# Kernel optimization log

Hardware: AMD Instinct MI355X
Metric: run time of the kernel (lower is better)

## Reference

```python
import jax, jax.numpy as jnp
import numpy as np
from jax import lax

SCALES = [4, 8, 16]
K_PER_SCALE = 4


def setup_inputs() -> dict:
    key = jax.random.key(0)
    B, N, D = 32, 4096, 384  # N = 64*64 perfect square
    features = jax.random.normal(key, (B, N, D), dtype=jnp.float32)
    return {"features": features}


def _kmeans_pp(feats, key, k):
    """k-means++ seeding on feats [N, D]; returns [k, D] centers.

    Faithful to torch version: first center uniform random, subsequent
    centers sampled with prob proportional to squared min distance
    (cdist is euclidean; probs = min_dist**2 == squared distance).
    Incremental min over squared distances is equivalent to recomputing
    cdist to all centers and taking the min each iteration.
    """
    N = feats.shape[0]
    k0, k1 = jax.random.split(key)
    idx0 = jax.random.randint(k0, (), 0, N)
    c0 = feats[idx0]  # [D]
    min_sq = jnp.sum((feats - c0) ** 2, axis=1)  # [N] squared dists

    def step(min_sq, kk):
        probs = min_sq / (min_sq.sum() + 1e-8)
        idx = jax.random.categorical(kk, jnp.log(probs + 1e-12))
        c = feats[idx]
        d = jnp.sum((feats - c) ** 2, axis=1)
        return jnp.minimum(min_sq, d), c

    keys = jax.random.split(k1, k - 1)
    _, rest = lax.scan(step, min_sq, keys)  # rest: [k-1, D]
    return jnp.concatenate([c0[None], rest], axis=0)


def reference(features):
    B, N, D = features.shape
    H = W = int(np.sqrt(N))
    x = features.reshape(B, H, W, D)
    base = jax.random.key(42)
    all_slots = []
    for si, s in enumerate(SCALES):
        # adaptive_avg_pool2d with H divisible by s == block mean
        pooled = x.reshape(B, s, H // s, s, W // s, D).mean(axis=(2, 4))  # [B,s,s,D]
        flat = pooled.reshape(B, s * s, D)
        bkeys = jax.random.split(jax.random.fold_in(base, si), B)
        cents = jax.vmap(lambda f, kk: _kmeans_pp(f, kk, K_PER_SCALE))(flat, bkeys)
        all_slots.append(cents)  # [B, k, D]
    return jnp.concatenate(all_slots, axis=1)  # [B, len(scales)*k, D]
```

## Files before the change

kernel.cpp:

```cpp
#include <hip/hip_runtime.h>
#include <stdint.h>

#define D_ 384
#define NPTS 4096
#define W4_OFF 0
#define W8_OFF 196608
#define W16_OFF 983040

__device__ __forceinline__ void tf_round(uint32_t& x0, uint32_t& x1, int r) {
  x0 += x1;
  x1 = (x1 << r) | (x1 >> (32 - r));
  x1 ^= x0;
}

__device__ void tf2x32(uint32_t k0, uint32_t k1, uint32_t x0, uint32_t x1,
                       uint32_t& y0, uint32_t& y1) {
  uint32_t ks2 = k0 ^ k1 ^ 0x1BD11BDAu;
  x0 += k0; x1 += k1;
  tf_round(x0, x1, 13); tf_round(x0, x1, 15); tf_round(x0, x1, 26); tf_round(x0, x1, 6);
  x0 += k1; x1 += ks2 + 1u;
  tf_round(x0, x1, 17); tf_round(x0, x1, 29); tf_round(x0, x1, 16); tf_round(x0, x1, 24);
  x0 += ks2; x1 += k0 + 2u;
  tf_round(x0, x1, 13); tf_round(x0, x1, 15); tf_round(x0, x1, 26); tf_round(x0, x1, 6);
  x0 += k0; x1 += k1 + 3u;
  tf_round(x0, x1, 17); tf_round(x0, x1, 29); tf_round(x0, x1, 16); tf_round(x0, x1, 24);
  x0 += k1; x1 += ks2 + 4u;
  tf_round(x0, x1, 13); tf_round(x0, x1, 15); tf_round(x0, x1, 26); tf_round(x0, x1, 6);
  x0 += ks2; x1 += k0 + 5u;
  y0 = x0; y1 = x1;
}

__global__ __launch_bounds__(384) void pool16_kernel(const float* __restrict__ feats,
                                                     float* __restrict__ ws) {
  int blk = blockIdx.x;
  int b = blk >> 6;
  int cell = ((blk & 63) << 2) + threadIdx.y;
  int q = threadIdx.x;
  int ch = cell >> 4, cw = cell & 15;
  const float* fb = feats + (size_t)b * NPTS * D_;
  float ax = 0.f, ay = 0.f, az = 0.f, aw = 0.f;
  #pragma unroll
  for (int dh = 0; dh < 4; ++dh) {
    int h = ch * 4 + dh;
    #pragma unroll
    for (int dw = 0; dw < 4; ++dw) {
      int w = cw * 4 + dw;
      float4 v = *(const float4*)(fb + ((size_t)(h * 64 + w)) * D_ + q * 4);
      ax += v.x; ay += v.y; az += v.z; aw += v.w;
    }
  }
  float4 o = { ax * (1.f/16.f), ay * (1.f/16.f), az * (1.f/16.f), aw * (1.f/16.f) };
  *(float4*)(ws + W16_OFF + ((size_t)(b * 256 + cell)) * D_ + q * 4) = o;
}

__global__ __launch_bounds__(256) void pool_rest_kernel(float* __restrict__ ws) {
  int gid = blockIdx.x * 256 + threadIdx.x;
  if (gid < 196608) {
    int q = gid % 96;
    int c8 = (gid / 96) & 63;
    int b = gid / (96 * 64);
    int p = c8 >> 3, r = c8 & 7;
    const float4* w16b = (const float4*)(ws + W16_OFF + (size_t)b * 256 * D_);
    float ax = 0.f, ay = 0.f, az = 0.f, aw = 0.f;
    #pragma unroll
    for (int a = 0; a < 2; ++a)
      #pragma unroll
      for (int c = 0; c < 2; ++c) {
        int cell = (p * 2 + a) * 16 + (r * 2 + c);
        float4 v = w16b[(size_t)cell * 96 + q];
        ax += v.x; ay += v.y; az += v.z; aw += v.w;
      }
    float4 o = { ax * 0.25f, ay * 0.25f, az * 0.25f, aw * 0.25f };
    *(float4*)(ws + W8_OFF + ((size_t)(b * 64 + c8)) * D_ + q * 4) = o;
  } else {
    int idx = gid - 196608;
    int q = idx % 96;
    int c4 = (idx / 96) & 15;
    int b = idx / (96 * 16);
    int p = c4 >> 2, r = c4 & 3;
    const float4* w16b = (const float4*)(ws + W16_OFF + (size_t)b * 256 * D_);
    float ax = 0.f, ay = 0.f, az = 0.f, aw = 0.f;
    #pragma unroll
    for (int a = 0; a < 2; ++a)
      #pragma unroll
      for (int c = 0; c < 2; ++c) {
        int p8 = p * 2 + a, r8 = r * 2 + c;
        float bx = 0.f, by = 0.f, bz = 0.f, bw = 0.f;
        #pragma unroll
        for (int a2 = 0; a2 < 2; ++a2)
          #pragma unroll
          for (int c2 = 0; c2 < 2; ++c2) {
            int cell = (p8 * 2 + a2) * 16 + (r8 * 2 + c2);
            float4 v = w16b[(size_t)cell * 96 + q];
            bx += v.x; by += v.y; bz += v.z; bw += v.w;
          }
        bx *= 0.25f; by *= 0.25f; bz *= 0.25f; bw *= 0.25f;
        ax += bx; ay += by; az += bz; aw += bw;
      }
    float4 o = { ax * 0.25f, ay * 0.25f, az * 0.25f, aw * 0.25f };
    *(float4*)(ws + W4_OFF + ((size_t)(b * 16 + c4)) * D_ + q * 4) = o;
  }
}

__global__ __launch_bounds__(512) void kmeans_kernel(const float* __restrict__ ws,
                                                     float* __restrict__ out) {
  int blk = blockIdx.x;
  int si = blk >> 5;
  int b  = blk & 31;
  int n  = (si == 0) ? 16 : (si == 1) ? 64 : 256;

  const float* pooled;
  if (si == 0)      pooled = ws + W4_OFF  + (size_t)b * 16  * D_;
  else if (si == 1) pooled = ws + W8_OFF  + (size_t)b * 64  * D_;
  else              pooled = ws + W16_OFF + (size_t)b * 256 * D_;
  float* ob = out + ((size_t)b * 12 + si * 4) * D_;

  __shared__ __align__(16) float4 csh4[98];
  __shared__ float minsq[256];
  __shared__ uint32_t skey[3][2];
  __shared__ int sidx0;
  __shared__ float wmaxv[4];
  __shared__ int   wmaxi[4];

  int tid  = threadIdx.x;
  int row  = tid >> 1;
  int part = tid & 1;
  int lane = tid & 63;
  int wv   = tid >> 6;

  float4 xr[48];
  if (row < n) {
    const float4* rp = (const float4*)(pooled + (size_t)row * D_ + part * 192);
    #pragma unroll
    for (int k = 0; k < 48; ++k) xr[k] = rp[k];
  }
  if (tid < 256) minsq[tid] = 0.f;

  if (tid < 64) {
    uint32_t f0, f1, bk0, bk1, r0, r1, s0, s1, e0, e1;
    tf2x32(0u, 42u, 0u, (uint32_t)si, f0, f1);
    tf2x32(f0, f1, 0u, (uint32_t)b, bk0, bk1);
    uint32_t cC = (tid < 3) ? 1u : 0u;
    tf2x32(bk0, bk1, 0u, cC, r0, r1);
    uint32_t cD = (tid < 3) ? (uint32_t)tid : 1u;
    tf2x32(r0, r1, 0u, cD, s0, s1);
    tf2x32(s0, s1, 0u, 0u, e0, e1);
    if (tid < 3) { skey[tid][0] = s0; skey[tid][1] = s1; }
    else if (tid == 3) sidx0 = (int)((e0 ^ e1) & (uint32_t)(n - 1));
  }
  __syncthreads();

  int s = sidx0;
  if (row == s) {
    float4* cb = csh4 + part * 49;
    float4* op = (float4*)(ob + part * 192);
    #pragma unroll
    for (int k = 0; k < 48; ++k) { cb[k] = xr[k]; op[k] = xr[k]; }
  }
  __syncthreads();

  if (row < n) {
    float acc = 0.f;
    #pragma unroll
    for (int k = 0; k < 48; ++k) {
      float4 c4 = csh4[part * 49 + k];
      float dx = xr[k].x - c4.x, dy = xr[k].y - c4.y;
      float dz = xr[k].z - c4.z, dw = xr[k].w - c4.w;
      acc += dx * dx; acc += dy * dy; acc += dz * dz; acc += dw * dw;
    }
    acc += __shfl_xor(acc, 1);
    if (part == 0) minsq[row] = acc;
  }
  __syncthreads();

  const float TINY = __uint_as_float(0x00800000u);

  #pragma unroll 1
  for (int t = 0; t < 3; ++t) {
    if (tid < 256) {
      float z = -1e30f;
      if (tid < n) {
        float m = minsq[tid];
        uint32_t y0, y1;
        tf2x32(skey[t][0], skey[t][1], 0u, (uint32_t)tid, y0, y1);
        uint32_t bits = y0 ^ y1;
        float f = __uint_as_float((bits >> 9) | 0x3F800000u) - 1.0f;
        float u = (f > 0.f) ? f : TINY;
        z = -__logf(-__logf(u)) + __logf(m);
      }
      float bv = z; int bi = tid;
      #pragma unroll
      for (int m2 = 1; m2 < 64; m2 <<= 1) {
        float ov = __shfl_xor(bv, m2);
        int   oi = __shfl_xor(bi, m2);
        if (ov > bv || (ov == bv && oi < bi)) { bv = ov; bi = oi; }
      }
      if (lane == 0) { wmaxv[wv] = bv; wmaxi[wv] = bi; }
    }
    __syncthreads();

    float cv = wmaxv[0]; int ci = wmaxi[0];
    #pragma unroll
    for (int w2 = 1; w2 < 4; ++w2)
      if (wmaxv[w2] > cv || (wmaxv[w2] == cv && wmaxi[w2] < ci)) { cv = wmaxv[w2]; ci = wmaxi[w2]; }
    s = ci;

    if (row == s) {
      float4* op = (float4*)(ob + (size_t)(t + 1) * D_ + part * 192);
      float4* cb = csh4 + part * 49;
      #pragma unroll
      for (int k = 0; k < 48; ++k) { op[k] = xr[k]; if (t < 2) cb[k] = xr[k]; }
    }
    if (t < 2) {
      __syncthreads();
      if (row < n) {
        float acc = 0.f;
        #pragma unroll
        for (int k = 0; k < 48; ++k) {
          float4 c4 = csh4[part * 49 + k];
          float dx = xr[k].x - c4.x, dy = xr[k].y - c4.y;
          float dz = xr[k].z - c4.z, dw = xr[k].w - c4.w;
          acc += dx * dx; acc += dy * dy; acc += dz * dz; acc += dw * dw;
        }
        acc += __shfl_xor(acc, 1);
        if (part == 0) minsq[row] = fminf(minsq[row], acc);
      }
      __syncthreads();
    }
  }
}

extern "C" void kernel_launch(void* const* d_in, const int* in_sizes, int n_in,
                              void* d_out, int out_size, void* d_ws, size_t ws_size,
                              hipStream_t stream) {
  const float* feats = (const float*)d_in[0];
  float* out = (float*)d_out;
  float* ws  = (float*)d_ws;

  pool16_kernel<<<2048, dim3(96, 4, 1), 0, stream>>>(feats, ws);
  pool_rest_kernel<<<960, 256, 0, stream>>>(ws);
  kmeans_kernel<<<96, 512, 0, stream>>>(ws, out);
}
```

Baseline: 63.52 us.

## Transpose pooled features to dim-major layout and split rows across four threads

Replaces the coarser-scale pooling kernel with one that transposes the 16x16 pooled features through shared memory into a dimension-major layout and builds the 8x8 and 4x4 pools from that tile. The k-means kernel now runs 1024 threads with four threads per point, each holding 96 scalars, and reads the transposed data so consecutive threads load consecutive addresses. The aim is to cut per-thread register pressure and the serial distance-loop length, and to make the register-load phase coalesced. In exchange it adds an extra full copy of the pooled data, scalar instead of vector loads, an extra shuffle step, and strided scalar stores of the chosen centers.

```diff
diff --git a/kernel.cpp b/kernel.cpp
--- a/kernel.cpp
+++ b/kernel.cpp
@@ -3,9 +3,10 @@
 
 #define D_ 384
 #define NPTS 4096
-#define W4_OFF 0
-#define W8_OFF 196608
-#define W16_OFF 983040
+#define W16_OFF  0
+#define W16T_OFF 3145728
+#define W8T_OFF  6291456
+#define W4T_OFF  7077888
 
 __device__ __forceinline__ void tf_round(uint32_t& x0, uint32_t& x1, int r) {
   x0 += x1;
@@ -53,69 +54,68 @@
   *(float4*)(ws + W16_OFF + ((size_t)(b * 256 + cell)) * D_ + q * 4) = o;
 }
 
-__global__ __launch_bounds__(256) void pool_rest_kernel(float* __restrict__ ws) {
-  int gid = blockIdx.x * 256 + threadIdx.x;
-  if (gid < 196608) {
-    int q = gid % 96;
-    int c8 = (gid / 96) & 63;
-    int b = gid / (96 * 64);
-    int p = c8 >> 3, r = c8 & 7;
-    const float4* w16b = (const float4*)(ws + W16_OFF + (size_t)b * 256 * D_);
-    float ax = 0.f, ay = 0.f, az = 0.f, aw = 0.f;
+__global__ __launch_bounds__(256) void transpose_pool_kernel(float* __restrict__ ws) {
+  int blk = blockIdx.x;
+  int b = blk / 12, slab = blk % 12;
+  int d0 = slab * 32;
+  const float* w16b = ws + W16_OFF + (size_t)b * 98304;
+  float* w16T = ws + W16T_OFF + (size_t)b * 98304;
+  float* w8T  = ws + W8T_OFF  + (size_t)b * 24576;
+  float* w4T  = ws + W4T_OFF  + (size_t)b * 6144;
+
+  __shared__ float T[32][257];
+  int t = threadIdx.x;
+  int x = t & 31, yc = t >> 5;
+
+  #pragma unroll
+  for (int c = yc; c < 256; c += 8)
+    T[x][c] = w16b[(size_t)c * 384 + d0 + x];
+  __syncthreads();
+
+  int c = t & 63, dq = t >> 6;
+  for (int dd = dq; dd < 32; dd += 4) {
+    #pragma unroll
+    for (int co = 0; co < 256; co += 64)
+      w16T[(size_t)(d0 + dd) * 256 + c + co] = T[dd][c + co];
+  }
+  for (int dd = dq; dd < 32; dd += 4) {
+    int p = c >> 3, r = c & 7;
+    int c00 = p * 32 + r * 2;
+    float v = ((T[dd][c00] + T[dd][c00 + 1]) + T[dd][c00 + 16]) + T[dd][c00 + 17];
+    w8T[(size_t)(d0 + dd) * 64 + c] = v * 0.25f;
+  }
+  int c4 = t & 15, dp = t >> 4;
+  for (int dd = dp; dd < 32; dd += 16) {
+    int p = c4 >> 2, r = c4 & 3;
+    float ax = 0.f;
     #pragma unroll
     for (int a = 0; a < 2; ++a)
       #pragma unroll
-      for (int c = 0; c < 2; ++c) {
-        int cell = (p * 2 + a) * 16 + (r * 2 + c);
-        float4 v = w16b[(size_t)cell * 96 + q];
-        ax += v.x; ay += v.y; az += v.z; aw += v.w;
-      }
-    float4 o = { ax * 0.25f, ay * 0.25f, az * 0.25f, aw * 0.25f };
-    *(float4*)(ws + W8_OFF + ((size_t)(b * 64 + c8)) * D_ + q * 4) = o;
-  } else {
-    int idx = gid - 196608;
-    int q = idx % 96;
-    int c4 = (idx / 96) & 15;
-    int b = idx / (96 * 16);
-    int p = c4 >> 2, r = c4 & 3;
-    const float4* w16b = (const float4*)(ws + W16_OFF + (size_t)b * 256 * D_);
-    float ax = 0.f, ay = 0.f, az = 0.f, aw = 0.f;
-    #pragma unroll
-    for (int a = 0; a < 2; ++a)
-      #pragma unroll
-      for (int c = 0; c < 2; ++c) {
-        int p8 = p * 2 + a, r8 = r * 2 + c;
-        float bx = 0.f, by = 0.f, bz = 0.f, bw = 0.f;
-        #pragma unroll
-        for (int a2 = 0; a2 < 2; ++a2)
-          #pragma unroll
-          for (int c2 = 0; c2 < 2; ++c2) {
-            int cell = (p8 * 2 + a2) * 16 + (r8 * 2 + c2);
-            float4 v = w16b[(size_t)cell * 96 + q];
-            bx += v.x; by += v.y; bz += v.z; bw += v.w;
-          }
-        bx *= 0.25f; by *= 0.25f; bz *= 0.25f; bw *= 0.25f;
-        ax += bx; ay += by; az += bz; aw += bw;
-      }
-    float4 o = { ax * 0.25f, ay * 0.25f, az * 0.25f, aw * 0.25f };
-    *(float4*)(ws + W4_OFF + ((size_t)(b * 16 + c4)) * D_ + q * 4) = o;
-  }
-}
-
-__global__ __launch_bounds__(512) void kmeans_kernel(const float* __restrict__ ws,
-                                                     float* __restrict__ out) {
+      for (int cc = 0; cc < 2; ++cc) {
+        int p8 = p * 2 + a, r8 = r * 2 + cc;
+        int cA = p8 * 32 + r8 * 2;
+        float bx = ((T[dd][cA] + T[dd][cA + 1]) + T[dd][cA + 16]) + T[dd][cA + 17];
+        ax += bx * 0.25f;
+      }
+    w4T[(size_t)(d0 + dd) * 16 + c4] = ax * 0.25f;
+  }
+}
+
+__global__ __launch_bounds__(1024) void kmeans_kernel(const float* __restrict__ ws,
+                                                      float* __restrict__ out) {
   int blk = blockIdx.x;
   int si = blk >> 5;
   int b  = blk & 31;
   int n  = (si == 0) ? 16 : (si == 1) ? 64 : 256;
 
-  const float* pooled;
-  if (si == 0)      pooled = ws + W4_OFF  + (size_t)b * 16  * D_;
-  else if (si == 1) pooled = ws + W8_OFF  + (size_t)b * 64  * D_;
-  else              pooled = ws + W16_OFF + (size_t)b * 256 * D_;
+  const float* pT;
+  int nc;
+  if (si == 0)      { pT = ws + W4T_OFF  + (size_t)b * 6144;  nc = 16;  }
+  else if (si == 1) { pT = ws + W8T_OFF  + (size_t)b * 24576; nc = 64;  }
+  else              { pT = ws + W16T_OFF + (size_t)b * 98304; nc = 256; }
   float* ob = out + ((size_t)b * 12 + si * 4) * D_;
 
-  __shared__ __align__(16) float4 csh4[98];
+  __shared__ float csh[4 * 97];
   __shared__ float minsq[256];
   __shared__ uint32_t skey[3][2];
   __shared__ int sidx0;
@@ -123,16 +123,16 @@
   __shared__ int   wmaxi[4];
 
   int tid  = threadIdx.x;
-  int row  = tid >> 1;
-  int part = tid & 1;
+  int row  = tid >> 2;
+  int part = tid & 3;
   int lane = tid & 63;
   int wv   = tid >> 6;
 
-  float4 xr[48];
+  float xr[96];
   if (row < n) {
-    const float4* rp = (const float4*)(pooled + (size_t)row * D_ + part * 192);
-    #pragma unroll
-    for (int k = 0; k < 48; ++k) xr[k] = rp[k];
+    const float* rp = pT + (size_t)(part * 96) * nc + row;
+    #pragma unroll
+    for (int j = 0; j < 96; ++j) xr[j] = rp[(size_t)j * nc];
   }
   if (tid < 256) minsq[tid] = 0.f;
 
@@ -152,23 +152,23 @@
 
   int s = sidx0;
   if (row == s) {
-    float4* cb = csh4 + part * 49;
-    float4* op = (float4*)(ob + part * 192);
-    #pragma unroll
-    for (int k = 0; k < 48; ++k) { cb[k] = xr[k]; op[k] = xr[k]; }
+    #pragma unroll
+    for (int j = 0; j < 96; ++j) {
+      csh[part * 97 + j] = xr[j];
+      ob[part * 96 + j] = xr[j];
+    }
   }
   __syncthreads();
 
   if (row < n) {
     float acc = 0.f;
     #pragma unroll
-    for (int k = 0; k < 48; ++k) {
-      float4 c4 = csh4[part * 49 + k];
-      float dx = xr[k].x - c4.x, dy = xr[k].y - c4.y;
-      float dz = xr[k].z - c4.z, dw = xr[k].w - c4.w;
-      acc += dx * dx; acc += dy * dy; acc += dz * dz; acc += dw * dw;
+    for (int j = 0; j < 96; ++j) {
+      float d = xr[j] - csh[part * 97 + j];
+      acc += d * d;
     }
     acc += __shfl_xor(acc, 1);
+    acc += __shfl_xor(acc, 2);
     if (part == 0) minsq[row] = acc;
   }
   __syncthreads();
@@ -206,23 +206,23 @@
     s = ci;
 
     if (row == s) {
-      float4* op = (float4*)(ob + (size_t)(t + 1) * D_ + part * 192);
-      float4* cb = csh4 + part * 49;
       #pragma unroll
-      for (int k = 0; k < 48; ++k) { op[k] = xr[k]; if (t < 2) cb[k] = xr[k]; }
+      for (int j = 0; j < 96; ++j) {
+        ob[(size_t)(t + 1) * D_ + part * 96 + j] = xr[j];
+        if (t < 2) csh[part * 97 + j] = xr[j];
+      }
     }
     if (t < 2) {
       __syncthreads();
       if (row < n) {
         float acc = 0.f;
         #pragma unroll
-        for (int k = 0; k < 48; ++k) {
-          float4 c4 = csh4[part * 49 + k];
-          float dx = xr[k].x - c4.x, dy = xr[k].y - c4.y;
-          float dz = xr[k].z - c4.z, dw = xr[k].w - c4.w;
-          acc += dx * dx; acc += dy * dy; acc += dz * dz; acc += dw * dw;
+        for (int j = 0; j < 96; ++j) {
+          float d = xr[j] - csh[part * 97 + j];
+          acc += d * d;
         }
         acc += __shfl_xor(acc, 1);
+        acc += __shfl_xor(acc, 2);
         if (part == 0) minsq[row] = fminf(minsq[row], acc);
       }
       __syncthreads();
@@ -238,6 +238,6 @@
   float* ws  = (float*)d_ws;
 
   pool16_kernel<<<2048, dim3(96, 4, 1), 0, stream>>>(feats, ws);
-  pool_rest_kernel<<<960, 256, 0, stream>>>(ws);
-  kmeans_kernel<<<96, 512, 0, stream>>>(ws, out);
-}
+  transpose_pool_kernel<<<384, 256, 0, stream>>>(ws);
+  kmeans_kernel<<<96, 1024, 0, stream>>>(ws, out);
+}
```

New measurement: 69.18 us. +8.9%, slower.

## Split k-means over many blocks with inter-block flag synchronization

Applied to the files above, without the earlier changes.

Replaces the 96-block k-means kernel with 448 blocks. Worker blocks each hold a 32-row slice of the pooled points in shared memory and compute distances and local argmax. Per-(scale,batch) coordinator blocks publish the chosen center and reduce the slice results, using atomic flags in global workspace. This spreads the serial k-means++ work across more CUs, at the cost of spin-wait handshakes. It also relies on all 448 blocks being co-resident, or the spin-waits can deadlock.

```diff
diff --git a/kernel.cpp b/kernel.cpp
--- a/kernel.cpp
+++ b/kernel.cpp
@@ -3,9 +3,16 @@
 
 #define D_ 384
 #define NPTS 4096
-#define W4_OFF 0
-#define W8_OFF 196608
-#define W16_OFF 983040
+#define W4_OFF   0
+#define W8_OFF   196608
+#define W16_OFF  983040
+#define CW_OFF   4128768
+#define ZV_OFF   4165632
+#define ZI_OFF   4166400
+#define FA_OFF   4167168
+#define FB_OFF   4167552
+
+#define AGENT __HIP_MEMORY_SCOPE_AGENT
 
 __device__ __forceinline__ void tf_round(uint32_t& x0, uint32_t& x1, int r) {
   x0 += x1;
@@ -54,6 +61,10 @@
 }
 
 __global__ __launch_bounds__(256) void pool_rest_kernel(float* __restrict__ ws) {
+  if (blockIdx.x == 0) {
+    int* iw = (int*)ws;
+    for (int i = threadIdx.x; i < 768; i += 256) iw[FA_OFF + i] = 0;
+  }
   int gid = blockIdx.x * 256 + threadIdx.x;
   if (gid < 196608) {
     int q = gid % 96;
@@ -102,131 +113,155 @@
   }
 }
 
-__global__ __launch_bounds__(512) void kmeans_kernel(const float* __restrict__ ws,
-                                                     float* __restrict__ out) {
+__global__ __launch_bounds__(256) void km_coop(float* __restrict__ ws,
+                                               float* __restrict__ out) {
   int blk = blockIdx.x;
-  int si = blk >> 5;
-  int b  = blk & 31;
-  int n  = (si == 0) ? 16 : (si == 1) ? 64 : 256;
-
-  const float* pooled;
-  if (si == 0)      pooled = ws + W4_OFF  + (size_t)b * 16  * D_;
-  else if (si == 1) pooled = ws + W8_OFF  + (size_t)b * 64  * D_;
-  else              pooled = ws + W16_OFF + (size_t)b * 256 * D_;
-  float* ob = out + ((size_t)b * 12 + si * 4) * D_;
-
-  __shared__ __align__(16) float4 csh4[98];
-  __shared__ float minsq[256];
+  int tid = threadIdx.x;
+  int* iws = (int*)ws;
+
+  if (blk >= 352) {
+    if (tid >= 64) return;
+    int pk = blk - 352;
+    int si = pk >> 5, b = pk & 31;
+    int bsi = si * 32 + b;
+    int n   = (si == 0) ? 16 : (si == 1) ? 64 : 256;
+    int nsl = (si == 2) ? 8 : (si == 1) ? 2 : 1;
+    const float* tier = ws + ((si == 0) ? (size_t)W4_OFF  + (size_t)b * 16  * D_
+                         : (si == 1) ? (size_t)W8_OFF  + (size_t)b * 64  * D_
+                                     : (size_t)W16_OFF + (size_t)b * 256 * D_);
+    float* cw = ws + CW_OFF + (size_t)bsi * D_;
+    float* ob = out + ((size_t)b * 12 + si * 4) * D_;
+    int* fA = iws + FA_OFF + bsi * 4;
+    int* fB = iws + FB_OFF + bsi * 4;
+
+    int s;
+    {
+      uint32_t f0, f1, bk0, bk1, r0, r1, s0, s1, e0, e1;
+      tf2x32(0u, 42u, 0u, (uint32_t)si, f0, f1);
+      tf2x32(f0, f1, 0u, (uint32_t)b, bk0, bk1);
+      uint32_t cC = (tid < 3) ? 1u : 0u;
+      tf2x32(bk0, bk1, 0u, cC, r0, r1);
+      uint32_t cD = (tid < 3) ? (uint32_t)tid : 1u;
+      tf2x32(r0, r1, 0u, cD, s0, s1);
+      tf2x32(s0, s1, 0u, 0u, e0, e1);
+      int cand = (int)((e0 ^ e1) & (uint32_t)(n - 1));
+      s = __shfl(cand, 3);
+    }
+
+    for (int t = 0; t < 4; ++t) {
+      for (int j = tid; j < D_; j += 64) {
+        float v = tier[(size_t)s * D_ + j];
+        ob[(size_t)t * D_ + j] = v;
+        if (t < 3) __hip_atomic_store(&cw[j], v, __ATOMIC_RELAXED, AGENT);
+      }
+      if (t == 3) break;
+      __threadfence();
+      if (tid == 0) __hip_atomic_store(&fB[t], 1, __ATOMIC_RELEASE, AGENT);
+      int snew = 0;
+      if (tid == 0) {
+        while (__hip_atomic_load(&fA[t], __ATOMIC_ACQUIRE, AGENT) < nsl)
+          __builtin_amdgcn_s_sleep(1);
+        float bz = -1e38f; int bi = 0;
+        for (int sl = 0; sl < nsl; ++sl) {
+          float zr = __hip_atomic_load(&ws[ZV_OFF + bsi * 8 + sl], __ATOMIC_RELAXED, AGENT);
+          int   ir = __hip_atomic_load(&iws[ZI_OFF + bsi * 8 + sl], __ATOMIC_RELAXED, AGENT);
+          if (sl == 0 || zr > bz || (zr == bz && ir < bi)) { bz = zr; bi = ir; }
+        }
+        snew = bi;
+      }
+      s = __shfl(snew, 0);
+    }
+    return;
+  }
+
+  int si, b, sl, rows;
+  if (blk < 256)      { si = 2; b = blk >> 3;          sl = blk & 7; rows = 32; }
+  else if (blk < 320) { si = 1; b = (blk - 256) >> 1;  sl = (blk - 256) & 1; rows = 32; }
+  else                { si = 0; b = blk - 320;         sl = 0; rows = 16; }
+  int bsi = si * 32 + b;
+  int rowbase = sl * 32;
+  const float* tier = ws + ((si == 0) ? (size_t)W4_OFF  + (size_t)b * 16  * D_
+                       : (si == 1) ? (size_t)W8_OFF  + (size_t)b * 64  * D_
+                                   : (size_t)W16_OFF + (size_t)b * 256 * D_);
+  const float* cw = ws + CW_OFF + (size_t)bsi * D_;
+  int* fA = iws + FA_OFF + bsi * 4;
+  int* fB = iws + FB_OFF + bsi * 4;
+
+  __shared__ float L[32][385];
+  __shared__ float csh[D_];
+  __shared__ float pc[8][33];
+  __shared__ float msq[32];
   __shared__ uint32_t skey[3][2];
-  __shared__ int sidx0;
-  __shared__ float wmaxv[4];
-  __shared__ int   wmaxi[4];
-
-  int tid  = threadIdx.x;
-  int row  = tid >> 1;
-  int part = tid & 1;
-  int lane = tid & 63;
-  int wv   = tid >> 6;
-
-  float4 xr[48];
-  if (row < n) {
-    const float4* rp = (const float4*)(pooled + (size_t)row * D_ + part * 192);
-    #pragma unroll
-    for (int k = 0; k < 48; ++k) xr[k] = rp[k];
-  }
-  if (tid < 256) minsq[tid] = 0.f;
-
+
+  for (int i = tid; i < rows * D_; i += 256) {
+    int r = i / D_, c = i - r * D_;
+    L[r][c] = tier[(size_t)(rowbase + r) * D_ + c];
+  }
   if (tid < 64) {
-    uint32_t f0, f1, bk0, bk1, r0, r1, s0, s1, e0, e1;
+    uint32_t f0, f1, bk0, bk1, r0, r1, s0, s1;
     tf2x32(0u, 42u, 0u, (uint32_t)si, f0, f1);
     tf2x32(f0, f1, 0u, (uint32_t)b, bk0, bk1);
     uint32_t cC = (tid < 3) ? 1u : 0u;
     tf2x32(bk0, bk1, 0u, cC, r0, r1);
     uint32_t cD = (tid < 3) ? (uint32_t)tid : 1u;
     tf2x32(r0, r1, 0u, cD, s0, s1);
-    tf2x32(s0, s1, 0u, 0u, e0, e1);
     if (tid < 3) { skey[tid][0] = s0; skey[tid][1] = s1; }
-    else if (tid == 3) sidx0 = (int)((e0 ^ e1) & (uint32_t)(n - 1));
   }
   __syncthreads();
 
-  int s = sidx0;
-  if (row == s) {
-    float4* cb = csh4 + part * 49;
-    float4* op = (float4*)(ob + part * 192);
-    #pragma unroll
-    for (int k = 0; k < 48; ++k) { cb[k] = xr[k]; op[k] = xr[k]; }
-  }
-  __syncthreads();
-
-  if (row < n) {
-    float acc = 0.f;
-    #pragma unroll
-    for (int k = 0; k < 48; ++k) {
-      float4 c4 = csh4[part * 49 + k];
-      float dx = xr[k].x - c4.x, dy = xr[k].y - c4.y;
-      float dz = xr[k].z - c4.z, dw = xr[k].w - c4.w;
-      acc += dx * dx; acc += dy * dy; acc += dz * dz; acc += dw * dw;
-    }
-    acc += __shfl_xor(acc, 1);
-    if (part == 0) minsq[row] = acc;
-  }
-  __syncthreads();
-
   const float TINY = __uint_as_float(0x00800000u);
+  int r = tid & 31, part = tid >> 5;
 
   #pragma unroll 1
   for (int t = 0; t < 3; ++t) {
-    if (tid < 256) {
-      float z = -1e30f;
-      if (tid < n) {
-        float m = minsq[tid];
+    if (tid == 0) {
+      while (__hip_atomic_load(&fB[t], __ATOMIC_ACQUIRE, AGENT) == 0)
+        __builtin_amdgcn_s_sleep(1);
+    }
+    __syncthreads();
+    if (tid < 64) {
+      for (int j = tid; j < D_; j += 64)
+        csh[j] = __hip_atomic_load(&cw[j], __ATOMIC_RELAXED, AGENT);
+    }
+    __syncthreads();
+    float acc = 0.f;
+    if (r < rows) {
+      #pragma unroll
+      for (int j = 0; j < 48; ++j) {
+        float d = L[r][part * 48 + j] - csh[part * 48 + j];
+        acc += d * d;
+      }
+    }
+    pc[part][r] = acc;
+    __syncthreads();
+    if (tid < 64) {
+      float z = -1e38f; int gi = rowbase + tid;
+      if (tid < rows) {
+        float d = ((pc[0][tid] + pc[1][tid]) + (pc[2][tid] + pc[3][tid]))
+                + ((pc[4][tid] + pc[5][tid]) + (pc[6][tid] + pc[7][tid]));
+        float m = (t == 0) ? d : fminf(msq[tid], d);
+        msq[tid] = m;
         uint32_t y0, y1;
-        tf2x32(skey[t][0], skey[t][1], 0u, (uint32_t)tid, y0, y1);
+        tf2x32(skey[t][0], skey[t][1], 0u, (uint32_t)gi, y0, y1);
         uint32_t bits = y0 ^ y1;
         float f = __uint_as_float((bits >> 9) | 0x3F800000u) - 1.0f;
         float u = (f > 0.f) ? f : TINY;
         z = -__logf(-__logf(u)) + __logf(m);
       }
-      float bv = z; int bi = tid;
+      float bv = z; int bi = gi;
       #pragma unroll
       for (int m2 = 1; m2 < 64; m2 <<= 1) {
         float ov = __shfl_xor(bv, m2);
         int   oi = __shfl_xor(bi, m2);
         if (ov > bv || (ov == bv && oi < bi)) { bv = ov; bi = oi; }
       }
-      if (lane == 0) { wmaxv[wv] = bv; wmaxi[wv] = bi; }
-    }
-    __syncthreads();
-
-    float cv = wmaxv[0]; int ci = wmaxi[0];
-    #pragma unroll
-    for (int w2 = 1; w2 < 4; ++w2)
-      if (wmaxv[w2] > cv || (wmaxv[w2] == cv && wmaxi[w2] < ci)) { cv = wmaxv[w2]; ci = wmaxi[w2]; }
-    s = ci;
-
-    if (row == s) {
-      float4* op = (float4*)(ob + (size_t)(t + 1) * D_ + part * 192);
-      float4* cb = csh4 + part * 49;
-      #pragma unroll
-      for (int k = 0; k < 48; ++k) { op[k] = xr[k]; if (t < 2) cb[k] = xr[k]; }
-    }
-    if (t < 2) {
-      __syncthreads();
-      if (row < n) {
-        float acc = 0.f;
-        #pragma unroll
-        for (int k = 0; k < 48; ++k) {
-          float4 c4 = csh4[part * 49 + k];
-          float dx = xr[k].x - c4.x, dy = xr[k].y - c4.y;
-          float dz = xr[k].z - c4.z, dw = xr[k].w - c4.w;
-          acc += dx * dx; acc += dy * dy; acc += dz * dz; acc += dw * dw;
-        }
-        acc += __shfl_xor(acc, 1);
-        if (part == 0) minsq[row] = fminf(minsq[row], acc);
-      }
-      __syncthreads();
-    }
+      if (tid == 0) {
+        __hip_atomic_store(&ws[ZV_OFF + bsi * 8 + sl], bv, __ATOMIC_RELAXED, AGENT);
+        __hip_atomic_store(&iws[ZI_OFF + bsi * 8 + sl], bi, __ATOMIC_RELAXED, AGENT);
+        __hip_atomic_fetch_add(&fA[t], 1, __ATOMIC_RELEASE, AGENT);
+      }
+    }
+    __syncthreads();
   }
 }
 
@@ -239,5 +274,5 @@
 
   pool16_kernel<<<2048, dim3(96, 4, 1), 0, stream>>>(feats, ws);
   pool_rest_kernel<<<960, 256, 0, stream>>>(ws);
-  kmeans_kernel<<<96, 512, 0, stream>>>(ws, out);
-}
+  km_coop<<<448, 256, 0, stream>>>(ws, out);
+}
```

After: 164.9 us. +159.5%, slower.
